# Optimization experiments

Measured on AMD Instinct MI355X. Metric: run time of the kernel, lower is better.

Reference implementation:

```python
import jax, jax.numpy as jnp
import numpy as np

VOCAB = 91557
WORD_DIM = 512
HIDDEN = 1024
B, T = 256, 128


def lstm_maxpool(x_emb, W_ih, W_hh, b_ih, b_hh):
    """x_emb: [B, T, D]. PyTorch LSTMCell recurrence (zero init state),
    then elementwise max over time of the hidden states."""
    Bq = x_emb.shape[0]
    H = W_hh.shape[1]

    def step(carry, x_t):
        h, c = carry
        gates = x_t @ W_ih.T + b_ih + h @ W_hh.T + b_hh  # [B, 4H]
        i, f, g, o = jnp.split(gates, 4, axis=-1)  # PyTorch gate order i,f,g,o
        i = jax.nn.sigmoid(i)
        f = jax.nn.sigmoid(f)
        g = jnp.tanh(g)
        o = jax.nn.sigmoid(o)
        c = f * c + i * g
        h = o * jnp.tanh(c)
        return (h, c), h

    h0 = jnp.zeros((Bq, H), x_emb.dtype)
    (_h, _c), hs = jax.lax.scan(step, (h0, h0), jnp.swapaxes(x_emb, 0, 1))  # hs: [T, B, H]
    return jnp.max(hs, axis=0)  # [B, H]


def setup_inputs() -> dict:
    key = jax.random.key(0)
    ks = jax.random.split(key, 9)
    question = jax.random.randint(ks[0], (B, T), 0, VOCAB)
    sentence = jax.random.randint(ks[1], (B, T), 0, VOCAB)
    emb = jax.random.normal(ks[2], (VOCAB, WORD_DIM), dtype=jnp.float32) * 0.02
    W_ih = jax.random.normal(ks[3], (4 * HIDDEN, WORD_DIM), dtype=jnp.float32) * 0.02
    W_hh = jax.random.normal(ks[4], (4 * HIDDEN, HIDDEN), dtype=jnp.float32) * 0.02
    b_ih = jax.random.normal(ks[5], (4 * HIDDEN,), dtype=jnp.float32) * 0.02
    b_hh = jax.random.normal(ks[6], (4 * HIDDEN,), dtype=jnp.float32) * 0.02
    W_last = jax.random.normal(ks[7], (2, 2 * HIDDEN), dtype=jnp.float32) * 0.02
    b_last = jax.random.normal(ks[8], (2,), dtype=jnp.float32) * 0.02
    return {
        "question": question, "sentence": sentence,
        "emb": emb, "W_ih": W_ih, "W_hh": W_hh, "b_ih": b_ih, "b_hh": b_hh,
        "W_last": W_last, "b_last": b_last,
    }


def reference(question, sentence, emb, W_ih, W_hh, b_ih, b_hh, W_last, b_last):
    q_embedded = emb[question]  # [B, T, D]
    s_embedded = emb[sentence]  # [B, T, D]
    hq = lstm_maxpool(q_embedded, W_ih, W_hh, b_ih, b_hh)  # [B, H]
    hs = lstm_maxpool(s_embedded, W_ih, W_hh, b_ih, b_hh)  # [B, H]
    out = jnp.concatenate([hq, hs], axis=1) @ W_last.T + b_last  # [B, 2]
    return jax.nn.sigmoid(out)
```

## Files before the change

### kernel.cpp

```cpp
#include <hip/hip_runtime.h>
#include <hip/hip_bf16.h>
#include <cstdint>


typedef __bf16 bf16x8 __attribute__((ext_vector_type(8)));
typedef float f32x4 __attribute__((ext_vector_type(4)));

__device__ __forceinline__ float sigm(float x) {
    return 1.0f / (1.0f + __expf(-x));
}
__device__ __forceinline__ float tanh_fast(float x) {
    x = fminf(15.0f, fmaxf(-15.0f, x));
    float e = __expf(2.0f * x);
    return (e - 1.0f) / (e + 1.0f);
}
__device__ __forceinline__ ushort f2bu(float f) {
    __hip_bfloat16 h = __float2bfloat16(f);
    return __builtin_bit_cast(unsigned short, h);
}

__global__ void prep_weights(const float* __restrict__ Wih,
                             const float* __restrict__ Whh,
                             const float* __restrict__ bih,
                             const float* __restrict__ bhh,
                             __hip_bfloat16* __restrict__ WcT,
                             float* __restrict__ biasc) {
    int p = blockIdx.y;
    int k = blockIdx.x * blockDim.x + threadIdx.x;
    int r = (p & 3) * 1024 + (p >> 2);
    float v = (k < 512) ? Wih[(size_t)r * 512 + k]
                        : Whh[(size_t)r * 1024 + (k - 512)];
    WcT[(size_t)p * 1536 + k] = __float2bfloat16(v);
    if (k == 0) biasc[p] = bih[r] + bhh[r];
}

__global__ void gather_embed(const int* __restrict__ q,
                             const int* __restrict__ s,
                             const float* __restrict__ emb,
                             ushort* __restrict__ X) {
    int rb = blockIdx.x;
    int t = rb >> 9;
    int b = rb & 511;
    int tok = (b < 256) ? q[b * 128 + t] : s[(b - 256) * 128 + t];
    const float2* src = (const float2*)(emb + (size_t)tok * 512);
    ushort2* dst = (ushort2*)(X + (size_t)rb * 512);
    float2 v = src[threadIdx.x];
    ushort2 o;
    o.x = f2bu(v.x);
    o.y = f2bu(v.y);
    dst[threadIdx.x] = o;
}

__global__ void init_state(float* __restrict__ C, float* __restrict__ HMAX,
                           ushort* __restrict__ H0) {
    int i = blockIdx.x * 256 + threadIdx.x;
    C[i] = 0.0f;
    HMAX[i] = -1e30f;
    H0[i] = 0;
}

__global__ __launch_bounds__(256, 2) void lstm_step(
    const ushort* __restrict__ X,
    const ushort* __restrict__ WcT,
    const float* __restrict__ biasc,
    const ushort* __restrict__ Hin,
    ushort* __restrict__ Hout,
    float* __restrict__ C,
    float* __restrict__ HMAX,
    int t) {
    __shared__ __align__(16) ushort As[64][72];
    __shared__ __align__(16) ushort Bs[64][72];
    __shared__ float Gs[64][68];
    __shared__ float biasS[64];

    const int tid = threadIdx.x;
    const int m0 = blockIdx.y * 64;
    const int n0 = blockIdx.x * 64;

    if (tid < 64) biasS[tid] = biasc[n0 + tid];

    const int lane = tid & 63;
    const int w = tid >> 6;
    const int quad = lane >> 4;
    const int l16 = lane & 15;
    const int wm = (w >> 1) * 32;
    const int wn = (w & 1) * 32;

    f32x4 acc[2][2] = {};

    const int r1 = tid >> 3;
    const int seg = (tid & 7) * 8;

    for (int it = 0; it < 24; ++it) {
        const int kk = it * 64 + seg;
        const ushort* a1;
        const ushort* a2;
        if (kk < 512) {
            const ushort* xbase = X + (size_t)(t * 512 + m0) * 512 + kk;
            a1 = xbase + (size_t)r1 * 512;
            a2 = xbase + (size_t)(r1 + 32) * 512;
        } else {
            const ushort* hbase = Hin + (size_t)m0 * 1024 + (kk - 512);
            a1 = hbase + (size_t)r1 * 1024;
            a2 = hbase + (size_t)(r1 + 32) * 1024;
        }
        const ushort* b1 = WcT + (size_t)(n0 + r1) * 1536 + kk;
        const ushort* b2 = WcT + (size_t)(n0 + r1 + 32) * 1536 + kk;
        uint4 va1 = *(const uint4*)a1;
        uint4 va2 = *(const uint4*)a2;
        uint4 vb1 = *(const uint4*)b1;
        uint4 vb2 = *(const uint4*)b2;
        __syncthreads();
        *(uint4*)&As[r1][seg] = va1;
        *(uint4*)&As[r1 + 32][seg] = va2;
        *(uint4*)&Bs[r1][seg] = vb1;
        *(uint4*)&Bs[r1 + 32][seg] = vb2;
        __syncthreads();
#pragma unroll
        for (int kc = 0; kc < 2; ++kc) {
            bf16x8 a0 = *(const bf16x8*)&As[wm + l16][kc * 32 + quad * 8];
            bf16x8 a1f = *(const bf16x8*)&As[wm + 16 + l16][kc * 32 + quad * 8];
            bf16x8 b0 = *(const bf16x8*)&Bs[wn + l16][kc * 32 + quad * 8];
            bf16x8 b1f = *(const bf16x8*)&Bs[wn + 16 + l16][kc * 32 + quad * 8];
            acc[0][0] = __builtin_amdgcn_mfma_f32_16x16x32_bf16(a0, b0, acc[0][0], 0, 0, 0);
            acc[0][1] = __builtin_amdgcn_mfma_f32_16x16x32_bf16(a0, b1f, acc[0][1], 0, 0, 0);
            acc[1][0] = __builtin_amdgcn_mfma_f32_16x16x32_bf16(a1f, b0, acc[1][0], 0, 0, 0);
            acc[1][1] = __builtin_amdgcn_mfma_f32_16x16x32_bf16(a1f, b1f, acc[1][1], 0, 0, 0);
        }
    }
    __syncthreads();

#pragma unroll
    for (int mt = 0; mt < 2; ++mt)
#pragma unroll
        for (int nt = 0; nt < 2; ++nt)
#pragma unroll
            for (int rg = 0; rg < 4; ++rg)
                Gs[wm + mt * 16 + quad * 4 + rg][wn + nt * 16 + l16] =
                    acc[mt][nt][rg];
    __syncthreads();

    const int m = tid >> 2;
    const int jb = (tid & 3) * 4;
    const size_t gbase = (size_t)(m0 + m) * 1024 + (n0 >> 2) + jb;

    f32x4 cold = *(const f32x4*)&C[gbase];
    f32x4 hm = *(const f32x4*)&HMAX[gbase];
    f32x4 cnew, hv;
#pragma unroll
    for (int u = 0; u < 4; ++u) {
        int jj = jb + u;
        float gi = Gs[m][4 * jj + 0] + biasS[4 * jj + 0];
        float gf = Gs[m][4 * jj + 1] + biasS[4 * jj + 1];
        float gg = Gs[m][4 * jj + 2] + biasS[4 * jj + 2];
        float go = Gs[m][4 * jj + 3] + biasS[4 * jj + 3];
        float iv = sigm(gi);
        float fv = sigm(gf);
        float gv = tanh_fast(gg);
        float ov = sigm(go);
        float cn = fv * cold[u] + iv * gv;
        float h = ov * tanh_fast(cn);
        cnew[u] = cn;
        hv[u] = h;
        hm[u] = fmaxf(hm[u], h);
    }
    *(f32x4*)&C[gbase] = cnew;
    *(f32x4*)&HMAX[gbase] = hm;
    ushort4 hb;
    hb.x = f2bu(hv[0]);
    hb.y = f2bu(hv[1]);
    hb.z = f2bu(hv[2]);
    hb.w = f2bu(hv[3]);
    *(ushort4*)&Hout[gbase] = hb;
}

__global__ void final_out(const float* __restrict__ HMAX,
                          const float* __restrict__ Wl,
                          const float* __restrict__ bl,
                          float* __restrict__ out) {
    int b = blockIdx.x;
    int tid = threadIdx.x;
    float s0 = 0.0f, s1 = 0.0f;
    for (int j = tid; j < 1024; j += 256) {
        float hq = HMAX[(size_t)b * 1024 + j];
        float hs = HMAX[(size_t)(256 + b) * 1024 + j];
        s0 += hq * Wl[j] + hs * Wl[1024 + j];
        s1 += hq * Wl[2048 + j] + hs * Wl[3072 + j];
    }
    __shared__ float r0[256], r1[256];
    r0[tid] = s0;
    r1[tid] = s1;
    __syncthreads();
    for (int off = 128; off > 0; off >>= 1) {
        if (tid < off) {
            r0[tid] += r0[tid + off];
            r1[tid] += r1[tid + off];
        }
        __syncthreads();
    }
    if (tid == 0) {
        out[b * 2 + 0] = sigm(r0[0] + bl[0]);
        out[b * 2 + 1] = sigm(r1[0] + bl[1]);
    }
}

extern "C" void kernel_launch(void* const* d_in, const int* in_sizes, int n_in,
                              void* d_out, int out_size, void* d_ws,
                              size_t ws_size, hipStream_t stream) {
    const int* q = (const int*)d_in[0];
    const int* s = (const int*)d_in[1];
    const float* emb = (const float*)d_in[2];
    const float* Wih = (const float*)d_in[3];
    const float* Whh = (const float*)d_in[4];
    const float* bih = (const float*)d_in[5];
    const float* bhh = (const float*)d_in[6];
    const float* Wl = (const float*)d_in[7];
    const float* bl = (const float*)d_in[8];
    float* out = (float*)d_out;

    char* ws = (char*)d_ws;
    __hip_bfloat16* WcT = (__hip_bfloat16*)(ws + 0);
    float* biasc = (float*)(ws + 12582912);
    ushort* X = (ushort*)(ws + 12599296);
    ushort* H0 = (ushort*)(ws + 79708160);
    ushort* H1 = (ushort*)(ws + 80756736);
    float* C = (float*)(ws + 81805312);
    float* HMAX = (float*)(ws + 83902464);

    prep_weights<<<dim3(6, 4096), 256, 0, stream>>>(Wih, Whh, bih, bhh, WcT,
                                                    biasc);
    gather_embed<<<65536, 256, 0, stream>>>(q, s, emb, X);
    init_state<<<2048, 256, 0, stream>>>(C, HMAX, H0);

    ushort* hin = H0;
    ushort* hout = H1;
    for (int t = 0; t < 128; ++t) {
        lstm_step<<<dim3(64, 8), 256, 0, stream>>>(X, (const ushort*)WcT, biasc,
                                                   hin, hout, C, HMAX, t);
        ushort* tmp = hin;
        hin = hout;
        hout = tmp;
    }
    final_out<<<256, 256, 0, stream>>>(HMAX, Wl, bl, out);
}
```

Baseline: 2.886 ms.

## Hoist input projection into chunked GEMM and widen recurrent step tiles

Splits the gate computation: the input projection x_t·W_ih is computed for 8 timesteps at a time by a separate large-tile GEMM into a bf16 buffer. Each per-step kernel then only does the recurrent h·W_hh product (K=1024 instead of 1536) and adds the precomputed projection. The change also uses 128-wide N tiles, direct global-to-LDS loads and swizzled LDS layouts. In exchange it adds an extra workspace buffer, a bf16 rounding of the input projection, and fewer blocks per step (256 instead of 512).

```diff
diff --git a/kernel.cpp b/kernel.cpp
--- a/kernel.cpp
+++ b/kernel.cpp
@@ -17,6 +17,14 @@
 __device__ __forceinline__ ushort f2bu(float f) {
     __hip_bfloat16 h = __float2bfloat16(f);
     return __builtin_bit_cast(unsigned short, h);
+}
+__device__ __forceinline__ float bu2f(ushort u) {
+    return __uint_as_float(((unsigned)u) << 16);
+}
+__device__ __forceinline__ void gl_lds16(const void* g, void* l) {
+    __builtin_amdgcn_global_load_lds(
+        (const __attribute__((address_space(1))) unsigned int*)g,
+        (__attribute__((address_space(3))) unsigned int*)l, 16, 0, 0);
 }
 
 __global__ void prep_weights(const float* __restrict__ Wih,
@@ -59,8 +67,73 @@
     H0[i] = 0;
 }
 
+__global__ __launch_bounds__(256, 2) void xproj_gemm(
+    const ushort* __restrict__ X,
+    const ushort* __restrict__ WcT,
+    ushort* __restrict__ Xb,
+    int row0) {
+    __shared__ __align__(16) ushort As[128 * 128];
+    __shared__ __align__(16) ushort Bs[128 * 128];
+
+    const int tid = threadIdx.x;
+    const int n0 = blockIdx.x * 128;
+    const int m0 = blockIdx.y * 128;
+    const int lane = tid & 63;
+    const int w = tid >> 6;
+    const int quad = lane >> 4;
+    const int l16 = lane & 15;
+    const int wm = (w >> 1) * 64;
+    const int wn = (w & 1) * 64;
+
+    f32x4 acc[4][4] = {};
+
+    for (int it = 0; it < 4; ++it) {
+        const int k0 = it * 128;
+        __syncthreads();
+#pragma unroll
+        for (int i = 0; i < 8; ++i) {
+            int u = i * 256 + tid;
+            int r = u >> 4;
+            int cs = (u & 15) ^ (r & 15);
+            gl_lds16(X + (size_t)(row0 + m0 + r) * 512 + k0 + cs * 8,
+                     (ushort*)As + (size_t)u * 8);
+            gl_lds16(WcT + (size_t)(n0 + r) * 1536 + k0 + cs * 8,
+                     (ushort*)Bs + (size_t)u * 8);
+        }
+        __syncthreads();
+#pragma unroll
+        for (int kb = 0; kb < 4; ++kb) {
+            bf16x8 af[4], bfr[4];
+            const int vsel = (kb << 2) | quad;
+#pragma unroll
+            for (int mi = 0; mi < 4; ++mi)
+                af[mi] = *(const bf16x8*)(As +
+                    (((wm + mi * 16 + l16) << 4) + (vsel ^ l16)) * 8);
+#pragma unroll
+            for (int ni = 0; ni < 4; ++ni)
+                bfr[ni] = *(const bf16x8*)(Bs +
+                    (((wn + ni * 16 + l16) << 4) + (vsel ^ l16)) * 8);
+#pragma unroll
+            for (int mi = 0; mi < 4; ++mi)
+#pragma unroll
+                for (int ni = 0; ni < 4; ++ni)
+                    acc[mi][ni] = __builtin_amdgcn_mfma_f32_16x16x32_bf16(
+                        af[mi], bfr[ni], acc[mi][ni], 0, 0, 0);
+        }
+    }
+
+#pragma unroll
+    for (int mi = 0; mi < 4; ++mi)
+#pragma unroll
+        for (int ni = 0; ni < 4; ++ni)
+#pragma unroll
+            for (int rg = 0; rg < 4; ++rg)
+                Xb[(size_t)(m0 + wm + mi * 16 + quad * 4 + rg) * 4096 +
+                   (n0 + wn + ni * 16 + l16)] = f2bu(acc[mi][ni][rg]);
+}
+
 __global__ __launch_bounds__(256, 2) void lstm_step(
-    const ushort* __restrict__ X,
+    const ushort* __restrict__ Xb,
     const ushort* __restrict__ WcT,
     const float* __restrict__ biasc,
     const ushort* __restrict__ Hin,
@@ -68,110 +141,122 @@
     float* __restrict__ C,
     float* __restrict__ HMAX,
     int t) {
-    __shared__ __align__(16) ushort As[64][72];
-    __shared__ __align__(16) ushort Bs[64][72];
-    __shared__ float Gs[64][68];
-    __shared__ float biasS[64];
+    __shared__ __align__(16) ushort As[64 * 128];
+    __shared__ __align__(16) ushort Bs[128 * 128];
+    __shared__ float Gs[64][132];
+    __shared__ float biasS[128];
 
     const int tid = threadIdx.x;
+    const int n0 = blockIdx.x * 128;
     const int m0 = blockIdx.y * 64;
-    const int n0 = blockIdx.x * 64;
-
-    if (tid < 64) biasS[tid] = biasc[n0 + tid];
+
+    if (tid < 128) biasS[tid] = biasc[n0 + tid];
 
     const int lane = tid & 63;
     const int w = tid >> 6;
     const int quad = lane >> 4;
     const int l16 = lane & 15;
     const int wm = (w >> 1) * 32;
-    const int wn = (w & 1) * 32;
-
-    f32x4 acc[2][2] = {};
-
-    const int r1 = tid >> 3;
-    const int seg = (tid & 7) * 8;
-
-    for (int it = 0; it < 24; ++it) {
-        const int kk = it * 64 + seg;
-        const ushort* a1;
-        const ushort* a2;
-        if (kk < 512) {
-            const ushort* xbase = X + (size_t)(t * 512 + m0) * 512 + kk;
-            a1 = xbase + (size_t)r1 * 512;
-            a2 = xbase + (size_t)(r1 + 32) * 512;
-        } else {
-            const ushort* hbase = Hin + (size_t)m0 * 1024 + (kk - 512);
-            a1 = hbase + (size_t)r1 * 1024;
-            a2 = hbase + (size_t)(r1 + 32) * 1024;
-        }
-        const ushort* b1 = WcT + (size_t)(n0 + r1) * 1536 + kk;
-        const ushort* b2 = WcT + (size_t)(n0 + r1 + 32) * 1536 + kk;
-        uint4 va1 = *(const uint4*)a1;
-        uint4 va2 = *(const uint4*)a2;
-        uint4 vb1 = *(const uint4*)b1;
-        uint4 vb2 = *(const uint4*)b2;
-        __syncthreads();
-        *(uint4*)&As[r1][seg] = va1;
-        *(uint4*)&As[r1 + 32][seg] = va2;
-        *(uint4*)&Bs[r1][seg] = vb1;
-        *(uint4*)&Bs[r1 + 32][seg] = vb2;
-        __syncthreads();
-#pragma unroll
-        for (int kc = 0; kc < 2; ++kc) {
-            bf16x8 a0 = *(const bf16x8*)&As[wm + l16][kc * 32 + quad * 8];
-            bf16x8 a1f = *(const bf16x8*)&As[wm + 16 + l16][kc * 32 + quad * 8];
-            bf16x8 b0 = *(const bf16x8*)&Bs[wn + l16][kc * 32 + quad * 8];
-            bf16x8 b1f = *(const bf16x8*)&Bs[wn + 16 + l16][kc * 32 + quad * 8];
-            acc[0][0] = __builtin_amdgcn_mfma_f32_16x16x32_bf16(a0, b0, acc[0][0], 0, 0, 0);
-            acc[0][1] = __builtin_amdgcn_mfma_f32_16x16x32_bf16(a0, b1f, acc[0][1], 0, 0, 0);
-            acc[1][0] = __builtin_amdgcn_mfma_f32_16x16x32_bf16(a1f, b0, acc[1][0], 0, 0, 0);
-            acc[1][1] = __builtin_amdgcn_mfma_f32_16x16x32_bf16(a1f, b1f, acc[1][1], 0, 0, 0);
-        }
-    }
+    const int wn = (w & 1) * 64;
+
+    f32x4 acc[2][4] = {};
+
+    for (int it = 0; it < 8; ++it) {
+        const int k0 = it * 128;
+        __syncthreads();
+#pragma unroll
+        for (int i = 0; i < 4; ++i) {
+            int u = i * 256 + tid;
+            int r = u >> 4;
+            int cs = (u & 15) ^ (r & 15);
+            gl_lds16(Hin + (size_t)(m0 + r) * 1024 + k0 + cs * 8,
+                     (ushort*)As + (size_t)u * 8);
+        }
+#pragma unroll
+        for (int i = 0; i < 8; ++i) {
+            int u = i * 256 + tid;
+            int r = u >> 4;
+            int cs = (u & 15) ^ (r & 15);
+            gl_lds16(WcT + (size_t)(n0 + r) * 1536 + 512 + k0 + cs * 8,
+                     (ushort*)Bs + (size_t)u * 8);
+        }
+        __syncthreads();
+#pragma unroll
+        for (int kb = 0; kb < 4; ++kb) {
+            bf16x8 af[2], bfr[4];
+            const int vsel = (kb << 2) | quad;
+#pragma unroll
+            for (int mi = 0; mi < 2; ++mi)
+                af[mi] = *(const bf16x8*)(As +
+                    (((wm + mi * 16 + l16) << 4) + (vsel ^ l16)) * 8);
+#pragma unroll
+            for (int ni = 0; ni < 4; ++ni)
+                bfr[ni] = *(const bf16x8*)(Bs +
+                    (((wn + ni * 16 + l16) << 4) + (vsel ^ l16)) * 8);
+#pragma unroll
+            for (int mi = 0; mi < 2; ++mi)
+#pragma unroll
+                for (int ni = 0; ni < 4; ++ni)
+                    acc[mi][ni] = __builtin_amdgcn_mfma_f32_16x16x32_bf16(
+                        af[mi], bfr[ni], acc[mi][ni], 0, 0, 0);
+        }
+    }
+
+#pragma unroll
+    for (int mi = 0; mi < 2; ++mi)
+#pragma unroll
+        for (int ni = 0; ni < 4; ++ni)
+#pragma unroll
+            for (int rg = 0; rg < 4; ++rg)
+                Gs[wm + mi * 16 + quad * 4 + rg][wn + ni * 16 + l16] =
+                    acc[mi][ni][rg];
     __syncthreads();
 
-#pragma unroll
-    for (int mt = 0; mt < 2; ++mt)
-#pragma unroll
-        for (int nt = 0; nt < 2; ++nt)
-#pragma unroll
-            for (int rg = 0; rg < 4; ++rg)
-                Gs[wm + mt * 16 + quad * 4 + rg][wn + nt * 16 + l16] =
-                    acc[mt][nt][rg];
-    __syncthreads();
-
     const int m = tid >> 2;
-    const int jb = (tid & 3) * 4;
-    const size_t gbase = (size_t)(m0 + m) * 1024 + (n0 >> 2) + jb;
-
-    f32x4 cold = *(const f32x4*)&C[gbase];
-    f32x4 hm = *(const f32x4*)&HMAX[gbase];
-    f32x4 cnew, hv;
-#pragma unroll
-    for (int u = 0; u < 4; ++u) {
-        int jj = jb + u;
-        float gi = Gs[m][4 * jj + 0] + biasS[4 * jj + 0];
-        float gf = Gs[m][4 * jj + 1] + biasS[4 * jj + 1];
-        float gg = Gs[m][4 * jj + 2] + biasS[4 * jj + 2];
-        float go = Gs[m][4 * jj + 3] + biasS[4 * jj + 3];
+    const int c4 = tid & 3;
+    const int col0 = c4 * 32;
+    const size_t hrow = (size_t)(m0 + m) * 1024;
+    const int j0 = (n0 >> 2) + c4 * 8;
+    const ushort* xp =
+        Xb + (size_t)((t & 7) * 512 + m0 + m) * 4096 + n0 + col0;
+
+    f32x4 cold0 = *(const f32x4*)&C[hrow + j0];
+    f32x4 cold1 = *(const f32x4*)&C[hrow + j0 + 4];
+    f32x4 hm0 = *(const f32x4*)&HMAX[hrow + j0];
+    f32x4 hm1 = *(const f32x4*)&HMAX[hrow + j0 + 4];
+    f32x4 cn0, cn1;
+    ushort4 hb0, hb1;
+#pragma unroll
+    for (int u = 0; u < 8; ++u) {
+        int cb = col0 + 4 * u;
+        float gi = Gs[m][cb + 0] + bu2f(xp[4 * u + 0]) + biasS[cb + 0];
+        float gf = Gs[m][cb + 1] + bu2f(xp[4 * u + 1]) + biasS[cb + 1];
+        float gg = Gs[m][cb + 2] + bu2f(xp[4 * u + 2]) + biasS[cb + 2];
+        float go = Gs[m][cb + 3] + bu2f(xp[4 * u + 3]) + biasS[cb + 3];
         float iv = sigm(gi);
         float fv = sigm(gf);
         float gv = tanh_fast(gg);
         float ov = sigm(go);
-        float cn = fv * cold[u] + iv * gv;
+        float cold = (u < 4) ? cold0[u & 3] : cold1[u & 3];
+        float cn = fv * cold + iv * gv;
         float h = ov * tanh_fast(cn);
-        cnew[u] = cn;
-        hv[u] = h;
-        hm[u] = fmaxf(hm[u], h);
-    }
-    *(f32x4*)&C[gbase] = cnew;
-    *(f32x4*)&HMAX[gbase] = hm;
-    ushort4 hb;
-    hb.x = f2bu(hv[0]);
-    hb.y = f2bu(hv[1]);
-    hb.z = f2bu(hv[2]);
-    hb.w = f2bu(hv[3]);
-    *(ushort4*)&Hout[gbase] = hb;
+        ushort hbits = f2bu(h);
+        if (u < 4) {
+            cn0[u & 3] = cn;
+            hm0[u & 3] = fmaxf(hm0[u & 3], h);
+            ((ushort*)&hb0)[u & 3] = hbits;
+        } else {
+            cn1[u & 3] = cn;
+            hm1[u & 3] = fmaxf(hm1[u & 3], h);
+            ((ushort*)&hb1)[u & 3] = hbits;
+        }
+    }
+    *(f32x4*)&C[hrow + j0] = cn0;
+    *(f32x4*)&C[hrow + j0 + 4] = cn1;
+    *(f32x4*)&HMAX[hrow + j0] = hm0;
+    *(f32x4*)&HMAX[hrow + j0 + 4] = hm1;
+    *(ushort4*)&Hout[hrow + j0] = hb0;
+    *(ushort4*)&Hout[hrow + j0 + 4] = hb1;
 }
 
 __global__ void final_out(const float* __restrict__ HMAX,
@@ -222,10 +307,11 @@
     __hip_bfloat16* WcT = (__hip_bfloat16*)(ws + 0);
     float* biasc = (float*)(ws + 12582912);
     ushort* X = (ushort*)(ws + 12599296);
-    ushort* H0 = (ushort*)(ws + 79708160);
-    ushort* H1 = (ushort*)(ws + 80756736);
-    float* C = (float*)(ws + 81805312);
-    float* HMAX = (float*)(ws + 83902464);
+    ushort* Xb = (ushort*)(ws + 79708160);
+    ushort* H0 = (ushort*)(ws + 113262592);
+    ushort* H1 = (ushort*)(ws + 114311168);
+    float* C = (float*)(ws + 115359744);
+    float* HMAX = (float*)(ws + 117456896);
 
     prep_weights<<<dim3(6, 4096), 256, 0, stream>>>(Wih, Whh, bih, bhh, WcT,
                                                     biasc);
@@ -234,12 +320,17 @@
 
     ushort* hin = H0;
     ushort* hout = H1;
-    for (int t = 0; t < 128; ++t) {
-        lstm_step<<<dim3(64, 8), 256, 0, stream>>>(X, (const ushort*)WcT, biasc,
-                                                   hin, hout, C, HMAX, t);
-        ushort* tmp = hin;
-        hin = hout;
-        hout = tmp;
+    for (int c = 0; c < 16; ++c) {
+        xproj_gemm<<<dim3(32, 32), 256, 0, stream>>>(X, (const ushort*)WcT, Xb,
+                                                     c * 4096);
+        for (int tt = 0; tt < 8; ++tt) {
+            int t = c * 8 + tt;
+            lstm_step<<<dim3(32, 8), 256, 0, stream>>>(
+                Xb, (const ushort*)WcT, biasc, hin, hout, C, HMAX, t);
+            ushort* tmp = hin;
+            hin = hout;
+            hout = tmp;
+        }
     }
     final_out<<<256, 256, 0, stream>>>(HMAX, Wl, bl, out);
 }
```

After: 2.496 ms. 1.16x faster.
